# Kernel optimization log

Hardware: AMD Instinct MI355X
Metric: run time of the kernel (lower is better)

## Reference

```python
import jax, jax.numpy as jnp
import numpy as np

N_NODES = 100000
F_DIM = 128      # graph.num_node_features
TE_DIM = 32      # te_emb_dim
D = F_DIM + TE_DIM  # attention embed_dim = 160
B = 4096         # number of target nodes (batched python loop)
K = 64           # candidates per target
TAU = 1.0
THRESHOLD = 0.2
EPS = 1e-10


def setup_inputs() -> dict:
    key = jax.random.key(0)
    ks = jax.random.split(key, 16)
    inp = {
        "x": jax.random.normal(ks[0], (N_NODES, F_DIM), dtype=jnp.float32),
        "target_node_ids": jax.random.randint(ks[1], (B,), 0, N_NODES),
        "target_node_times": jax.random.randint(ks[2], (B,), 1, 10000),
        "neighbor_ids": jax.random.randint(ks[3], (B, K), 0, N_NODES),
        "edge_time": jax.random.randint(ks[4], (B, K), 0, 10000),
        "edge_weight": jax.random.uniform(ks[5], (B, K), dtype=jnp.float32),
        "gumbel_u": jax.random.uniform(ks[6], (B, K), dtype=jnp.float32),
        # TemporalEncoding params: te(t) = cos(t * w + b)
        "te_w": jax.random.normal(ks[7], (TE_DIM,), dtype=jnp.float32),
        "te_b": jax.random.normal(ks[8], (TE_DIM,), dtype=jnp.float32),
        # MultiheadAttention params (packed qkv like torch)
        "in_proj_w": jax.random.normal(ks[9], (3 * D, D), dtype=jnp.float32) / np.sqrt(D),
        "in_proj_b": jnp.zeros((3 * D,), dtype=jnp.float32),
        "out_w": jax.random.normal(ks[10], (D, D), dtype=jnp.float32) / np.sqrt(D),
        "out_b": jnp.zeros((D,), dtype=jnp.float32),
        # MLP: Linear(D+1 -> 1) + LeakyReLU
        "mlp_w": jax.random.normal(ks[11], (D + 1,), dtype=jnp.float32) / np.sqrt(D + 1),
        "mlp_b": jnp.zeros((1,), dtype=jnp.float32),
    }
    return inp


def reference(x, target_node_ids, target_node_times, neighbor_ids, edge_time,
              edge_weight, gumbel_u, te_w, te_b, in_proj_w, in_proj_b,
              out_w, out_b, mlp_w, mlp_b):
    # --- build target embedding: [B, D]
    t_x = x[target_node_ids]                                          # [B, F]
    t_te = jnp.cos(target_node_times[:, None].astype(jnp.float32) * te_w + te_b)  # [B, TE]
    q_in = jnp.concatenate([t_x, t_te], axis=-1)                      # [B, D]

    # --- candidate embeddings: [B, K, D]
    c_x = x[neighbor_ids]                                             # [B, K, F]
    c_te = jnp.cos(edge_time[..., None].astype(jnp.float32) * te_w + te_b)        # [B, K, TE]
    kv_in = jnp.concatenate([c_x, c_te], axis=-1)                     # [B, K, D]

    # --- single-head MultiheadAttention (eval mode, 1 query per target)
    Wq, Wk, Wv = in_proj_w[:D], in_proj_w[D:2 * D], in_proj_w[2 * D:]
    bq, bk, bv = in_proj_b[:D], in_proj_b[D:2 * D], in_proj_b[2 * D:]
    q = q_in @ Wq.T + bq                                              # [B, D]
    k = jnp.einsum('bkf,df->bkd', kv_in, Wk) + bk                     # [B, K, D]
    v = jnp.einsum('bkf,df->bkd', kv_in, Wv) + bv                     # [B, K, D]
    scores = jnp.einsum('bd,bkd->bk', q, k) / jnp.sqrt(jnp.float32(D))
    attn_w = jax.nn.softmax(scores, axis=-1)                          # [B, K]
    ctx = jnp.einsum('bk,bkd->bd', attn_w, v)                         # [B, D]
    attn_output = ctx @ out_w.T + out_b                               # [B, D]

    # --- gumbel-softmax mask over attention weights (soft, then threshold)
    g = -jnp.log(-jnp.log(gumbel_u + EPS) + EPS)                      # gumbel(0,1)
    y_soft = jax.nn.softmax((attn_w + g) / TAU, axis=-1)
    candidate_mask = y_soft > THRESHOLD                               # [B, K] bool

    # --- MLP edge-weight update: Linear(D+1 -> 1) + LeakyReLU
    mlp_in = jnp.concatenate(
        [jnp.broadcast_to(attn_output[:, None, :], (attn_output.shape[0], edge_weight.shape[1], attn_output.shape[1])),
         edge_weight[..., None]], axis=-1)                            # [B, K, D+1]
    new_edge_weight = jax.nn.leaky_relu(jnp.einsum('bkf,f->bk', mlp_in, mlp_w) + mlp_b[0])  # [B, K]

    return attn_output, new_edge_weight, candidate_mask
```

## Files before the change

kernel.cpp:

```cpp
#include <hip/hip_runtime.h>

#define F_DIM 128
#define TE_DIM 32
#define DD 160
#define NB 4096
#define KK 64
#define ROWS 2
#define LD 164
#define TE_STRIDE 36
#define XH_STRIDE 132

#define WS_M   0
#define WS_V2  25600
#define WS_C   51200
#define WS_U   51360
#define WS_B2  51520
#define WS_S0  51680
#define WS_TE  51684
#define TAB_T  10000
#define TAB_N  (TAB_T * TE_DIM)
#define TAB_BLOCKS 250
#define SETUP_BASE (2 * DD + 3)

__device__ __forceinline__ float dot4acc(const float4 w, const float4 v, float a) {
    a = fmaf(w.x, v.x, a);
    a = fmaf(w.y, v.y, a);
    a = fmaf(w.z, v.z, a);
    a = fmaf(w.w, v.w, a);
    return a;
}

__device__ __forceinline__ float wave_max(float v) {
    #pragma unroll
    for (int off = 32; off > 0; off >>= 1) v = fmaxf(v, __shfl_xor(v, off, 64));
    return v;
}
__device__ __forceinline__ float wave_sum(float v) {
    #pragma unroll
    for (int off = 32; off > 0; off >>= 1) v += __shfl_xor(v, off, 64);
    return v;
}

__device__ __forceinline__ void gemv2r(
    const float* __restrict__ W, const float* __restrict__ bias,
    const float (*vin)[LD], float (*vout)[LD], int tid)
{
    const int r  = tid & 1;
    const int dl = tid >> 1;
    const float4* v4 = (const float4*)vin[r];
    const float4* w0 = (const float4*)(W + (long)dl * DD);
    float a0 = bias[dl];
    if (dl < 32) {
        const float4* w1 = (const float4*)(W + (long)(dl + 128) * DD);
        float a1 = bias[dl + 128];
        #pragma unroll 8
        for (int f = 0; f < 40; ++f) {
            const float4 v = v4[f];
            a0 = dot4acc(w0[f], v, a0);
            a1 = dot4acc(w1[f], v, a1);
        }
        vout[r][dl]       = a0;
        vout[r][dl + 128] = a1;
    } else {
        #pragma unroll 8
        for (int f = 0; f < 40; ++f) {
            const float4 v = v4[f];
            a0 = dot4acc(w0[f], v, a0);
        }
        vout[r][dl] = a0;
    }
}

__device__ __forceinline__ void gemv2r_sum2(
    const float* __restrict__ W, const float* __restrict__ bias,
    const float (*vin)[2][LD], float (*vout)[LD], int tid)
{
    const int r  = tid & 1;
    const int dl = tid >> 1;
    const float4* va = (const float4*)vin[r][0];
    const float4* vb = (const float4*)vin[r][1];
    const float4* w0 = (const float4*)(W + (long)dl * DD);
    float a0 = bias[dl];
    if (dl < 32) {
        const float4* w1 = (const float4*)(W + (long)(dl + 128) * DD);
        float a1 = bias[dl + 128];
        #pragma unroll 8
        for (int f = 0; f < 40; ++f) {
            const float4 A = va[f], B = vb[f];
            float4 v; v.x = A.x + B.x; v.y = A.y + B.y; v.z = A.z + B.z; v.w = A.w + B.w;
            a0 = dot4acc(w0[f], v, a0);
            a1 = dot4acc(w1[f], v, a1);
        }
        vout[r][dl]       = a0;
        vout[r][dl + 128] = a1;
    } else {
        #pragma unroll 8
        for (int f = 0; f < 40; ++f) {
            const float4 A = va[f], B = vb[f];
            float4 v; v.x = A.x + B.x; v.y = A.y + B.y; v.z = A.z + B.z; v.w = A.w + B.w;
            a0 = dot4acc(w0[f], v, a0);
        }
        vout[r][dl] = a0;
    }
}

__global__ __launch_bounds__(256)
void setup_kernel(const float* __restrict__ ipw, const float* __restrict__ ipb,
                  const float* __restrict__ ow,  const float* __restrict__ ob,
                  const float* __restrict__ te_w, const float* __restrict__ te_b,
                  float* __restrict__ ws)
{
    const int blk = blockIdx.x;
    const int t   = threadIdx.x;
    const float inv = 0.07905694150420949f;

    __shared__ float s_vec[DD];

    if (blk >= SETUP_BASE) {
        const int g0 = (blk - SETUP_BASE) * 256 + t;
        #pragma unroll
        for (int it = 0; it < 5; ++it) {
            const int g = g0 + it * (TAB_BLOCKS * 256);
            const int tt = g >> 5, d = g & 31;
            ws[WS_TE + g] = cosf(fmaf((float)tt, te_w[d], te_b[d]));
        }
        return;
    }

    if (blk < DD) {
        const float* wk = ipw + DD * DD;
        if (t < DD) s_vec[t] = wk[(long)t * DD + blk];
        __syncthreads();
        if (t < DD) {
            float a0 = 0.f, a1 = 0.f, a2 = 0.f, a3 = 0.f;
            #pragma unroll 4
            for (int d = 0; d < DD; d += 4) {
                a0 = fmaf(s_vec[d],     ipw[(long)d * DD + t],       a0);
                a1 = fmaf(s_vec[d + 1], ipw[(long)(d + 1) * DD + t], a1);
                a2 = fmaf(s_vec[d + 2], ipw[(long)(d + 2) * DD + t], a2);
                a3 = fmaf(s_vec[d + 3], ipw[(long)(d + 3) * DD + t], a3);
            }
            ws[WS_M + blk * DD + t] = (a0 + a1 + a2 + a3) * inv;
        }
    } else if (blk < 2 * DD) {
        const int i = blk - DD;
        const float* wv = ipw + 2 * DD * DD;
        if (t < DD) s_vec[t] = ow[(long)i * DD + t];
        __syncthreads();
        if (t < DD) {
            float a0 = 0.f, a1 = 0.f, a2 = 0.f, a3 = 0.f;
            #pragma unroll 4
            for (int d = 0; d < DD; d += 4) {
                a0 = fmaf(s_vec[d],     wv[(long)d * DD + t],       a0);
                a1 = fmaf(s_vec[d + 1], wv[(long)(d + 1) * DD + t], a1);
                a2 = fmaf(s_vec[d + 2], wv[(long)(d + 2) * DD + t], a2);
                a3 = fmaf(s_vec[d + 3], wv[(long)(d + 3) * DD + t], a3);
            }
            ws[WS_V2 + i * DD + t] = a0 + a1 + a2 + a3;
        }
    } else if (blk == 2 * DD) {
        const float* wk = ipw + DD * DD;
        if (t < DD) s_vec[t] = ipb[t];
        __syncthreads();
        if (t < DD) {
            float a0 = 0.f, a1 = 0.f, a2 = 0.f, a3 = 0.f;
            #pragma unroll 4
            for (int d = 0; d < DD; d += 4) {
                a0 = fmaf(s_vec[d],     wk[(long)d * DD + t],       a0);
                a1 = fmaf(s_vec[d + 1], wk[(long)(d + 1) * DD + t], a1);
                a2 = fmaf(s_vec[d + 2], wk[(long)(d + 2) * DD + t], a2);
                a3 = fmaf(s_vec[d + 3], wk[(long)(d + 3) * DD + t], a3);
            }
            ws[WS_C + t] = (a0 + a1 + a2 + a3) * inv;
        }
    } else if (blk == 2 * DD + 1) {
        if (t < DD) s_vec[t] = ipb[DD + t];
        __syncthreads();
        if (t < DD) {
            float a0 = 0.f, a1 = 0.f, a2 = 0.f, a3 = 0.f;
            #pragma unroll 4
            for (int d = 0; d < DD; d += 4) {
                a0 = fmaf(s_vec[d],     ipw[(long)d * DD + t],       a0);
                a1 = fmaf(s_vec[d + 1], ipw[(long)(d + 1) * DD + t], a1);
                a2 = fmaf(s_vec[d + 2], ipw[(long)(d + 2) * DD + t], a2);
                a3 = fmaf(s_vec[d + 3], ipw[(long)(d + 3) * DD + t], a3);
            }
            ws[WS_U + t] = (a0 + a1 + a2 + a3) * inv;
        }
    } else {
        if (t < DD) s_vec[t] = ipb[2 * DD + t];
        __syncthreads();
        if (t < DD) {
            const float* owr = ow + (long)t * DD;
            float a0 = 0.f, a1 = 0.f, a2 = 0.f, a3 = 0.f;
            #pragma unroll 4
            for (int d = 0; d < DD; d += 4) {
                a0 = fmaf(s_vec[d],     owr[d],     a0);
                a1 = fmaf(s_vec[d + 1], owr[d + 1], a1);
                a2 = fmaf(s_vec[d + 2], owr[d + 2], a2);
                a3 = fmaf(s_vec[d + 3], owr[d + 3], a3);
            }
            ws[WS_B2 + t] = ob[t] + (a0 + a1 + a2 + a3);
        }
        if (t >= 192) {
            const int lane = t - 192;
            float p = ipb[lane] * ipb[DD + lane];
            p = fmaf(ipb[lane + 64], ipb[DD + lane + 64], p);
            if (lane < 32) p = fmaf(ipb[lane + 128], ipb[DD + lane + 128], p);
            const float s = wave_sum(p);
            if (lane == 0) ws[WS_S0] = s * inv;
        }
    }
}

__global__ __launch_bounds__(256, 4)
void structure_learner_kernel(
    const float* __restrict__ x,
    const int*   __restrict__ target_node_ids,
    const int*   __restrict__ target_node_times,
    const int*   __restrict__ neighbor_ids,
    const int*   __restrict__ edge_time,
    const float* __restrict__ edge_weight,
    const float* __restrict__ gumbel_u,
    const float* __restrict__ te_w,
    const float* __restrict__ te_b,
    const float* __restrict__ mlp_w,
    const float* __restrict__ mlp_b,
    const float* __restrict__ ws,
    const float* __restrict__ tetab,
    float* __restrict__ out_ao,
    float* __restrict__ out_new,
    float* __restrict__ out_mask)
{
    __shared__ __attribute__((aligned(16))) _Float16 s_xh[ROWS][KK][XH_STRIDE];
    __shared__ __attribute__((aligned(16))) float s_qin[ROWS][LD];
    __shared__ __attribute__((aligned(16))) float s_qt[ROWS][LD];
    __shared__ __attribute__((aligned(16))) float s_wkvh[ROWS][2][LD];
    __shared__ __attribute__((aligned(16))) float s_ao[ROWS][LD];
    __shared__ float s_scp[ROWS][2][KK];
    __shared__ float s_attnw[ROWS][2][KK];
    __shared__ int   s_nid[ROWS][KK];
    __shared__ __attribute__((aligned(4))) _Float16 s_te[ROWS][KK][TE_STRIDE];

    const int tid  = threadIdx.x;
    const int w    = tid >> 6;
    const int lane = tid & 63;
    const int r    = w >> 1;
    const int h    = w & 1;
    const int b    = blockIdx.x * ROWS + r;

    const float* Mw = ws + WS_M;
    const float* V2 = ws + WS_V2;
    const float* Cv = ws + WS_C;
    const float* Uv = ws + WS_U;
    const float* B2 = ws + WS_B2;
    const float  s0 = ws[WS_S0];

    {
        if (h == 0) {
            s_nid[r][lane] = neighbor_ids[(long)b * KK + lane];
            const int tn = target_node_ids[b];
            const float2 tx = *(const float2*)(x + (long)tn * F_DIM + lane * 2);
            s_qin[r][lane * 2]     = tx.x;
            s_qin[r][lane * 2 + 1] = tx.y;
        } else if (lane < TE_DIM) {
            const int tt = target_node_times[b];
            s_qin[r][F_DIM + lane] =
                (tetab && (unsigned)tt < (unsigned)TAB_T)
                    ? tetab[(long)tt * TE_DIM + lane]
                    : cosf(fmaf((float)tt, te_w[lane], te_b[lane]));
        }
        const int q = lane >> 1, j = lane & 1;
        const int k = 32 * h + q;
        const int etv_i = edge_time[(long)b * KK + k];
        if (tetab && (unsigned)etv_i < (unsigned)TAB_T) {
            const float4* trow = (const float4*)(tetab + (long)etv_i * TE_DIM);
            #pragma unroll
            for (int q4 = 0; q4 < 4; ++q4) {
                const int jj = 4 * j + q4;
                const float4 tv = trow[jj];
                union { _Float16 h2[2]; unsigned u; } p0, p1;
                p0.h2[0] = (_Float16)tv.x; p0.h2[1] = (_Float16)tv.y;
                p1.h2[0] = (_Float16)tv.z; p1.h2[1] = (_Float16)tv.w;
                *(unsigned*)&s_te[r][k][4 * jj]     = p0.u;
                *(unsigned*)&s_te[r][k][4 * jj + 2] = p1.u;
            }
        } else {
            const float etv = (float)etv_i;
            #pragma unroll
            for (int ii = 0; ii < 8; ++ii) {
                const int d0 = 16 * j + 2 * ii;
                union { _Float16 h2[2]; unsigned u; } pk;
                pk.h2[0] = (_Float16)cosf(fmaf(etv, te_w[d0],     te_b[d0]));
                pk.h2[1] = (_Float16)cosf(fmaf(etv, te_w[d0 + 1], te_b[d0 + 1]));
                *(unsigned*)&s_te[r][k][d0] = pk.u;
            }
        }
    }
    __syncthreads();

    gemv2r(Mw, Cv, s_qin, s_qt, tid);
    __syncthreads();

    {
        float acc0 = 0.f, acc1 = 0.f;
        const int nidk = s_nid[r][lane];
        const float4* xr  = (const float4*)(x + (long)nidk * F_DIM + 64 * h);
        const float4* qt4 = (const float4*)(s_qt[r] + 64 * h);
        _Float16* st = &s_xh[r][lane][64 * h];
        #pragma unroll
        for (int f = 0; f < 16; f += 2) {
            const float4 a = xr[f], c = xr[f + 1];
            acc0 = dot4acc(a, qt4[f],     acc0);
            acc1 = dot4acc(c, qt4[f + 1], acc1);
            union { _Float16 hh[4]; unsigned long long u; } pa, pb;
            pa.hh[0] = (_Float16)a.x; pa.hh[1] = (_Float16)a.y;
            pa.hh[2] = (_Float16)a.z; pa.hh[3] = (_Float16)a.w;
            pb.hh[0] = (_Float16)c.x; pb.hh[1] = (_Float16)c.y;
            pb.hh[2] = (_Float16)c.z; pb.hh[3] = (_Float16)c.w;
            *(unsigned long long*)&st[4 * f]     = pa.u;
            *(unsigned long long*)&st[4 * f + 4] = pb.u;
        }
        float acc = acc0 + acc1;
        if (h == 0) {
            const float* qte = s_qt[r] + F_DIM;
            #pragma unroll
            for (int jj = 0; jj < 16; ++jj) {
                union { _Float16 h2[2]; unsigned u; } pk;
                pk.u = *(const unsigned*)&s_te[r][lane][2 * jj];
                acc = fmaf(qte[2 * jj],     (float)pk.h2[0], acc);
                acc = fmaf(qte[2 * jj + 1], (float)pk.h2[1], acc);
            }
            float p = s_qin[r][lane] * Uv[lane];
            p = fmaf(s_qin[r][lane + 64], Uv[lane + 64], p);
            if (lane < 32) p = fmaf(s_qin[r][128 + lane], Uv[128 + lane], p);
            acc += wave_sum(p) + s0;
        }
        s_scp[r][h][lane] = acc;
    }
    __syncthreads();

    float aw;
    {
        const float sc = s_scp[r][0][lane] + s_scp[r][1][lane];
        const float m = wave_max(sc);
        const float e = expf(sc - m);
        const float l = wave_sum(e);
        aw = e / l;
        s_attnw[r][h][lane] = aw;
    }

    {
        float ax = 0.f, ay = 0.f, at = 0.f;
        const int lte = lane & 31;
        #pragma unroll 8
        for (int qq = 0; qq < 32; ++qq) {
            const int kq = 32 * h + qq;
            const float wgt = s_attnw[r][h][kq];
            union { unsigned u; _Float16 h2[2]; } c;
            c.u = *(const unsigned*)&s_xh[r][kq][2 * lane];
            ax = fmaf(wgt, (float)c.h2[0], ax);
            ay = fmaf(wgt, (float)c.h2[1], ay);
            at = fmaf(wgt, (float)s_te[r][kq][lte], at);
        }
        s_wkvh[r][h][lane * 2]     = ax;
        s_wkvh[r][h][lane * 2 + 1] = ay;
        if (lane < TE_DIM) s_wkvh[r][h][F_DIM + lane] = at;
    }
    __syncthreads();

    float u = 0.f, ew = 0.f;
    if (h == 0) {
        u  = gumbel_u[(long)b * KK + lane];
        ew = edge_weight[(long)b * KK + lane];
    }

    gemv2r_sum2(V2, B2, s_wkvh, s_ao, tid);
    __syncthreads();

    if (h == 0) {
        float p = s_ao[r][lane] * mlp_w[lane];
        p = fmaf(s_ao[r][lane + 64], mlp_w[lane + 64], p);
        if (lane < 32) p = fmaf(s_ao[r][lane + 128], mlp_w[lane + 128], p);
        const float base = wave_sum(p) + mlp_b[0];

        float* ao = out_ao + (long)b * DD;
        ao[lane]      = s_ao[r][lane];
        ao[lane + 64] = s_ao[r][lane + 64];
        if (lane < 32) ao[lane + 128] = s_ao[r][lane + 128];

        const float g = -logf(-logf(u + 1e-10f) + 1e-10f);
        const float z = aw + g;
        const float m = wave_max(z);
        const float e = expf(z - m);
        const float l = wave_sum(e);
        out_mask[(long)b * KK + lane] = (e / l > 0.2f) ? 1.0f : 0.0f;

        const float val = fmaf(ew, mlp_w[DD], base);
        out_new[(long)b * KK + lane] = (val >= 0.f) ? val : 0.01f * val;
    }
}

extern "C" void kernel_launch(void* const* d_in, const int* in_sizes, int n_in,
                              void* d_out, int out_size, void* d_ws, size_t ws_size,
                              hipStream_t stream) {
    const float* x   = (const float*)d_in[0];
    const int*   tni = (const int*)d_in[1];
    const int*   tnt = (const int*)d_in[2];
    const int*   nid = (const int*)d_in[3];
    const int*   et  = (const int*)d_in[4];
    const float* ew  = (const float*)d_in[5];
    const float* gu  = (const float*)d_in[6];
    const float* tew = (const float*)d_in[7];
    const float* teb = (const float*)d_in[8];
    const float* ipw = (const float*)d_in[9];
    const float* ipb = (const float*)d_in[10];
    const float* ow  = (const float*)d_in[11];
    const float* ob  = (const float*)d_in[12];
    const float* mw  = (const float*)d_in[13];
    const float* mb  = (const float*)d_in[14];

    float* wsf = (float*)d_ws;

    float* out      = (float*)d_out;
    float* out_ao   = out;
    float* out_new  = out + (long)NB * DD;
    float* out_mask = out + (long)NB * DD + (long)NB * KK;

    const bool use_tab = ws_size >= (size_t)(WS_TE + TAB_N) * sizeof(float);
    const int  setup_grid = SETUP_BASE + (use_tab ? TAB_BLOCKS : 0);

    setup_kernel<<<setup_grid, 256, 0, stream>>>(ipw, ipb, ow, ob, tew, teb, wsf);

    structure_learner_kernel<<<NB / ROWS, 256, 0, stream>>>(
        x, tni, tnt, nid, et, ew, gu, tew, teb, mw, mb, wsf,
        use_tab ? (wsf + WS_TE) : nullptr,
        out_ao, out_new, out_mask);
}
```

Baseline: 181.9 us.

## Process one target per block with four waves splitting the feature dimension

Each 256-thread block now handles a single target row instead of two, and the four waves split the 128 candidate features into 32-wide slices. Partial scores and weighted-value sums are reduced across four waves through shared memory. The grid doubles to 4096 blocks, occupancy is raised to 5 via launch bounds, and the half-precision staging stride is padded to reduce bank conflicts. The trade-off is that only 160 of 256 threads work in the two GEMV stages, and the projection weights are re-read per target rather than shared across two rows.

```diff
diff --git a/kernel.cpp b/kernel.cpp
--- a/kernel.cpp
+++ b/kernel.cpp
@@ -5,10 +5,9 @@
 #define DD 160
 #define NB 4096
 #define KK 64
-#define ROWS 2
 #define LD 164
 #define TE_STRIDE 36
-#define XH_STRIDE 132
+#define XH_STRIDE 134
 
 #define WS_M   0
 #define WS_V2  25600
@@ -41,69 +40,6 @@
     return v;
 }
 
-__device__ __forceinline__ void gemv2r(
-    const float* __restrict__ W, const float* __restrict__ bias,
-    const float (*vin)[LD], float (*vout)[LD], int tid)
-{
-    const int r  = tid & 1;
-    const int dl = tid >> 1;
-    const float4* v4 = (const float4*)vin[r];
-    const float4* w0 = (const float4*)(W + (long)dl * DD);
-    float a0 = bias[dl];
-    if (dl < 32) {
-        const float4* w1 = (const float4*)(W + (long)(dl + 128) * DD);
-        float a1 = bias[dl + 128];
-        #pragma unroll 8
-        for (int f = 0; f < 40; ++f) {
-            const float4 v = v4[f];
-            a0 = dot4acc(w0[f], v, a0);
-            a1 = dot4acc(w1[f], v, a1);
-        }
-        vout[r][dl]       = a0;
-        vout[r][dl + 128] = a1;
-    } else {
-        #pragma unroll 8
-        for (int f = 0; f < 40; ++f) {
-            const float4 v = v4[f];
-            a0 = dot4acc(w0[f], v, a0);
-        }
-        vout[r][dl] = a0;
-    }
-}
-
-__device__ __forceinline__ void gemv2r_sum2(
-    const float* __restrict__ W, const float* __restrict__ bias,
-    const float (*vin)[2][LD], float (*vout)[LD], int tid)
-{
-    const int r  = tid & 1;
-    const int dl = tid >> 1;
-    const float4* va = (const float4*)vin[r][0];
-    const float4* vb = (const float4*)vin[r][1];
-    const float4* w0 = (const float4*)(W + (long)dl * DD);
-    float a0 = bias[dl];
-    if (dl < 32) {
-        const float4* w1 = (const float4*)(W + (long)(dl + 128) * DD);
-        float a1 = bias[dl + 128];
-        #pragma unroll 8
-        for (int f = 0; f < 40; ++f) {
-            const float4 A = va[f], B = vb[f];
-            float4 v; v.x = A.x + B.x; v.y = A.y + B.y; v.z = A.z + B.z; v.w = A.w + B.w;
-            a0 = dot4acc(w0[f], v, a0);
-            a1 = dot4acc(w1[f], v, a1);
-        }
-        vout[r][dl]       = a0;
-        vout[r][dl + 128] = a1;
-    } else {
-        #pragma unroll 8
-        for (int f = 0; f < 40; ++f) {
-            const float4 A = va[f], B = vb[f];
-            float4 v; v.x = A.x + B.x; v.y = A.y + B.y; v.z = A.z + B.z; v.w = A.w + B.w;
-            a0 = dot4acc(w0[f], v, a0);
-        }
-        vout[r][dl] = a0;
-    }
-}
-
 __global__ __launch_bounds__(256)
 void setup_kernel(const float* __restrict__ ipw, const float* __restrict__ ipb,
                   const float* __restrict__ ow,  const float* __restrict__ ob,
@@ -213,7 +149,7 @@
     }
 }
 
-__global__ __launch_bounds__(256, 4)
+__global__ __launch_bounds__(256, 5)
 void structure_learner_kernel(
     const float* __restrict__ x,
     const int*   __restrict__ target_node_ids,
@@ -232,22 +168,19 @@
     float* __restrict__ out_new,
     float* __restrict__ out_mask)
 {
-    __shared__ __attribute__((aligned(16))) _Float16 s_xh[ROWS][KK][XH_STRIDE];
-    __shared__ __attribute__((aligned(16))) float s_qin[ROWS][LD];
-    __shared__ __attribute__((aligned(16))) float s_qt[ROWS][LD];
-    __shared__ __attribute__((aligned(16))) float s_wkvh[ROWS][2][LD];
-    __shared__ __attribute__((aligned(16))) float s_ao[ROWS][LD];
-    __shared__ float s_scp[ROWS][2][KK];
-    __shared__ float s_attnw[ROWS][2][KK];
-    __shared__ int   s_nid[ROWS][KK];
-    __shared__ __attribute__((aligned(4))) _Float16 s_te[ROWS][KK][TE_STRIDE];
+    __shared__ __attribute__((aligned(16))) _Float16 s_xh[KK][XH_STRIDE];
+    __shared__ __attribute__((aligned(16))) float s_qin[LD];
+    __shared__ __attribute__((aligned(16))) float s_qt[LD];
+    __shared__ __attribute__((aligned(16))) float s_wkvp[4][LD];
+    __shared__ __attribute__((aligned(16))) float s_ao[LD];
+    __shared__ float s_scp[4][KK];
+    __shared__ float s_attnw[4][KK];
+    __shared__ __attribute__((aligned(4))) _Float16 s_te[KK][TE_STRIDE];
 
     const int tid  = threadIdx.x;
     const int w    = tid >> 6;
     const int lane = tid & 63;
-    const int r    = w >> 1;
-    const int h    = w & 1;
-    const int b    = blockIdx.x * ROWS + r;
+    const int b    = blockIdx.x;
 
     const float* Mw = ws + WS_M;
     const float* V2 = ws + WS_V2;
@@ -256,60 +189,67 @@
     const float* B2 = ws + WS_B2;
     const float  s0 = ws[WS_S0];
 
+    const int nid_l = neighbor_ids[(long)b * KK + lane];
+
     {
-        if (h == 0) {
-            s_nid[r][lane] = neighbor_ids[(long)b * KK + lane];
+        if (w == 0) {
             const int tn = target_node_ids[b];
             const float2 tx = *(const float2*)(x + (long)tn * F_DIM + lane * 2);
-            s_qin[r][lane * 2]     = tx.x;
-            s_qin[r][lane * 2 + 1] = tx.y;
-        } else if (lane < TE_DIM) {
+            s_qin[lane * 2]     = tx.x;
+            s_qin[lane * 2 + 1] = tx.y;
+        } else if (w == 1 && lane < TE_DIM) {
             const int tt = target_node_times[b];
-            s_qin[r][F_DIM + lane] =
+            s_qin[F_DIM + lane] =
                 (tetab && (unsigned)tt < (unsigned)TAB_T)
                     ? tetab[(long)tt * TE_DIM + lane]
                     : cosf(fmaf((float)tt, te_w[lane], te_b[lane]));
         }
-        const int q = lane >> 1, j = lane & 1;
-        const int k = 32 * h + q;
+        const int k = tid >> 2, j = tid & 3;
         const int etv_i = edge_time[(long)b * KK + k];
         if (tetab && (unsigned)etv_i < (unsigned)TAB_T) {
-            const float4* trow = (const float4*)(tetab + (long)etv_i * TE_DIM);
-            #pragma unroll
-            for (int q4 = 0; q4 < 4; ++q4) {
-                const int jj = 4 * j + q4;
-                const float4 tv = trow[jj];
-                union { _Float16 h2[2]; unsigned u; } p0, p1;
-                p0.h2[0] = (_Float16)tv.x; p0.h2[1] = (_Float16)tv.y;
-                p1.h2[0] = (_Float16)tv.z; p1.h2[1] = (_Float16)tv.w;
-                *(unsigned*)&s_te[r][k][4 * jj]     = p0.u;
-                *(unsigned*)&s_te[r][k][4 * jj + 2] = p1.u;
-            }
+            const float4* trow = (const float4*)(tetab + (long)etv_i * TE_DIM) + 2 * j;
+            const float4 t0 = trow[0], t1 = trow[1];
+            union { _Float16 h2[2]; unsigned u; } p0, p1, p2, p3;
+            p0.h2[0] = (_Float16)t0.x; p0.h2[1] = (_Float16)t0.y;
+            p1.h2[0] = (_Float16)t0.z; p1.h2[1] = (_Float16)t0.w;
+            p2.h2[0] = (_Float16)t1.x; p2.h2[1] = (_Float16)t1.y;
+            p3.h2[0] = (_Float16)t1.z; p3.h2[1] = (_Float16)t1.w;
+            *(unsigned*)&s_te[k][8 * j]     = p0.u;
+            *(unsigned*)&s_te[k][8 * j + 2] = p1.u;
+            *(unsigned*)&s_te[k][8 * j + 4] = p2.u;
+            *(unsigned*)&s_te[k][8 * j + 6] = p3.u;
         } else {
             const float etv = (float)etv_i;
             #pragma unroll
-            for (int ii = 0; ii < 8; ++ii) {
-                const int d0 = 16 * j + 2 * ii;
+            for (int ii = 0; ii < 4; ++ii) {
+                const int d0 = 8 * j + 2 * ii;
                 union { _Float16 h2[2]; unsigned u; } pk;
                 pk.h2[0] = (_Float16)cosf(fmaf(etv, te_w[d0],     te_b[d0]));
                 pk.h2[1] = (_Float16)cosf(fmaf(etv, te_w[d0 + 1], te_b[d0 + 1]));
-                *(unsigned*)&s_te[r][k][d0] = pk.u;
-            }
-        }
-    }
-    __syncthreads();
-
-    gemv2r(Mw, Cv, s_qin, s_qt, tid);
+                *(unsigned*)&s_te[k][d0] = pk.u;
+            }
+        }
+    }
+    __syncthreads();
+
+    if (tid < DD) {
+        const float4* v4   = (const float4*)s_qin;
+        const float4* wrow = (const float4*)(Mw + (long)tid * DD);
+        float a0 = Cv[tid];
+        #pragma unroll 8
+        for (int f = 0; f < 40; ++f) a0 = dot4acc(wrow[f], v4[f], a0);
+        s_qt[tid] = a0;
+    }
     __syncthreads();
 
     {
+        const int fo = 32 * w;
+        const float4* xr  = (const float4*)(x + (long)nid_l * F_DIM + fo);
+        const float4* qt4 = (const float4*)(s_qt + fo);
+        _Float16* st = &s_xh[lane][fo];
         float acc0 = 0.f, acc1 = 0.f;
-        const int nidk = s_nid[r][lane];
-        const float4* xr  = (const float4*)(x + (long)nidk * F_DIM + 64 * h);
-        const float4* qt4 = (const float4*)(s_qt[r] + 64 * h);
-        _Float16* st = &s_xh[r][lane][64 * h];
         #pragma unroll
-        for (int f = 0; f < 16; f += 2) {
+        for (int f = 0; f < 8; f += 2) {
             const float4 a = xr[f], c = xr[f + 1];
             acc0 = dot4acc(a, qt4[f],     acc0);
             acc1 = dot4acc(c, qt4[f + 1], acc1);
@@ -322,72 +262,91 @@
             *(unsigned long long*)&st[4 * f + 4] = pb.u;
         }
         float acc = acc0 + acc1;
-        if (h == 0) {
-            const float* qte = s_qt[r] + F_DIM;
+        if (w == 0) {
+            const float* qte = s_qt + F_DIM;
             #pragma unroll
             for (int jj = 0; jj < 16; ++jj) {
                 union { _Float16 h2[2]; unsigned u; } pk;
-                pk.u = *(const unsigned*)&s_te[r][lane][2 * jj];
+                pk.u = *(const unsigned*)&s_te[lane][2 * jj];
                 acc = fmaf(qte[2 * jj],     (float)pk.h2[0], acc);
                 acc = fmaf(qte[2 * jj + 1], (float)pk.h2[1], acc);
             }
-            float p = s_qin[r][lane] * Uv[lane];
-            p = fmaf(s_qin[r][lane + 64], Uv[lane + 64], p);
-            if (lane < 32) p = fmaf(s_qin[r][128 + lane], Uv[128 + lane], p);
+            float p = s_qin[lane] * Uv[lane];
+            p = fmaf(s_qin[lane + 64], Uv[lane + 64], p);
+            if (lane < 32) p = fmaf(s_qin[128 + lane], Uv[128 + lane], p);
             acc += wave_sum(p) + s0;
         }
-        s_scp[r][h][lane] = acc;
+        s_scp[w][lane] = acc;
     }
     __syncthreads();
 
     float aw;
     {
-        const float sc = s_scp[r][0][lane] + s_scp[r][1][lane];
+        const float sc = s_scp[0][lane] + s_scp[1][lane]
+                       + s_scp[2][lane] + s_scp[3][lane];
         const float m = wave_max(sc);
         const float e = expf(sc - m);
         const float l = wave_sum(e);
         aw = e / l;
-        s_attnw[r][h][lane] = aw;
+        s_attnw[w][lane] = aw;
     }
 
     {
         float ax = 0.f, ay = 0.f, at = 0.f;
         const int lte = lane & 31;
-        #pragma unroll 8
-        for (int qq = 0; qq < 32; ++qq) {
-            const int kq = 32 * h + qq;
-            const float wgt = s_attnw[r][h][kq];
+        #pragma unroll
+        for (int q = 0; q < 16; ++q) {
+            const int kq = 16 * w + q;
+            const float wgt = s_attnw[w][kq];
             union { unsigned u; _Float16 h2[2]; } c;
-            c.u = *(const unsigned*)&s_xh[r][kq][2 * lane];
+            c.u = *(const unsigned*)&s_xh[kq][2 * lane];
             ax = fmaf(wgt, (float)c.h2[0], ax);
             ay = fmaf(wgt, (float)c.h2[1], ay);
-            at = fmaf(wgt, (float)s_te[r][kq][lte], at);
-        }
-        s_wkvh[r][h][lane * 2]     = ax;
-        s_wkvh[r][h][lane * 2 + 1] = ay;
-        if (lane < TE_DIM) s_wkvh[r][h][F_DIM + lane] = at;
+            at = fmaf(wgt, (float)s_te[kq][lte], at);
+        }
+        s_wkvp[w][lane * 2]     = ax;
+        s_wkvp[w][lane * 2 + 1] = ay;
+        if (lane < TE_DIM) s_wkvp[w][F_DIM + lane] = at;
     }
     __syncthreads();
 
     float u = 0.f, ew = 0.f;
-    if (h == 0) {
+    if (w == 0) {
         u  = gumbel_u[(long)b * KK + lane];
         ew = edge_weight[(long)b * KK + lane];
     }
 
-    gemv2r_sum2(V2, B2, s_wkvh, s_ao, tid);
-    __syncthreads();
-
-    if (h == 0) {
-        float p = s_ao[r][lane] * mlp_w[lane];
-        p = fmaf(s_ao[r][lane + 64], mlp_w[lane + 64], p);
-        if (lane < 32) p = fmaf(s_ao[r][lane + 128], mlp_w[lane + 128], p);
+    if (tid < DD) {
+        const float4* wrow = (const float4*)(V2 + (long)tid * DD);
+        const float4* p0 = (const float4*)s_wkvp[0];
+        const float4* p1 = (const float4*)s_wkvp[1];
+        const float4* p2 = (const float4*)s_wkvp[2];
+        const float4* p3 = (const float4*)s_wkvp[3];
+        float a0 = B2[tid];
+        #pragma unroll 4
+        for (int f = 0; f < 40; ++f) {
+            const float4 A = p0[f], Bv = p1[f], C = p2[f], Dv = p3[f];
+            float4 v;
+            v.x = (A.x + Bv.x) + (C.x + Dv.x);
+            v.y = (A.y + Bv.y) + (C.y + Dv.y);
+            v.z = (A.z + Bv.z) + (C.z + Dv.z);
+            v.w = (A.w + Bv.w) + (C.w + Dv.w);
+            a0 = dot4acc(wrow[f], v, a0);
+        }
+        s_ao[tid] = a0;
+    }
+    __syncthreads();
+
+    if (w == 0) {
+        float p = s_ao[lane] * mlp_w[lane];
+        p = fmaf(s_ao[lane + 64], mlp_w[lane + 64], p);
+        if (lane < 32) p = fmaf(s_ao[lane + 128], mlp_w[lane + 128], p);
         const float base = wave_sum(p) + mlp_b[0];
 
         float* ao = out_ao + (long)b * DD;
-        ao[lane]      = s_ao[r][lane];
-        ao[lane + 64] = s_ao[r][lane + 64];
-        if (lane < 32) ao[lane + 128] = s_ao[r][lane + 128];
+        ao[lane]      = s_ao[lane];
+        ao[lane + 64] = s_ao[lane + 64];
+        if (lane < 32) ao[lane + 128] = s_ao[lane + 128];
 
         const float g = -logf(-logf(u + 1e-10f) + 1e-10f);
         const float z = aw + g;
@@ -432,7 +391,7 @@
 
     setup_kernel<<<setup_grid, 256, 0, stream>>>(ipw, ipb, ow, ob, tew, teb, wsf);
 
-    structure_learner_kernel<<<NB / ROWS, 256, 0, stream>>>(
+    structure_learner_kernel<<<NB, 256, 0, stream>>>(
         x, tni, tnt, nid, et, ew, gu, tew, teb, mw, mb, wsf,
         use_tab ? (wsf + WS_TE) : nullptr,
         out_ao, out_new, out_mask);
```

New measurement: 231.9 us. 27.5% more time.
